# Kernel optimization log

Hardware: AMD Instinct MI355X
Metric: run time of the kernel (lower is better)

## Reference

```python
import jax, jax.numpy as jnp
import numpy as np

N = 20000        # atoms
NEIGH = 12       # neighbors per atom
BSTEPS = 40      # bond GBF steps, range [0, 8]
ASTEPS = 20      # angle GBF steps, range [-1, 1]
H = 64           # hidden size
NCLS = 2         # n_classification
NCRYS = 20       # crystals (contiguous blocks of 1000 atoms)
NREL = 3         # edge relation types


def gbf(data, dmin, dmax, steps):
    # Gaussian basis expansion: exp(-(d - mu)^2 / gamma^2), gamma = (max-min)/steps
    filters = jnp.linspace(dmin, dmax, steps)
    gamma = (dmax - dmin) / steps
    return jnp.exp(-((data[..., None] - filters) ** 2) / gamma ** 2)


def rgcn(x, src, dst, etype, W_rel, W_root, b):
    # RGCNConv (PyG default): out = x @ W_root + b + sum_r mean_{j in N_r(i)} x_j @ W_r
    out = x @ W_root + b
    for r in range(NREL):
        w = (etype == r).astype(x.dtype)                     # [E]
        msg = (x @ W_rel[r])[src] * w[:, None]               # transform-then-gather: [E, H]
        s = jax.ops.segment_sum(msg, dst, num_segments=x.shape[0])
        c = jax.ops.segment_sum(w, dst, num_segments=x.shape[0])
        out = out + s / jnp.maximum(c, 1.0)[:, None]
    return out


def _forward(bond_fea, angle_fea, species, nbr_idx, crys_idx,
             W1b_rel, W1b_root, b1b, W1a_rel, W1a_root, b1a,
             W2b_rel, W2b_root, b2b, W2a_rel, W2a_root, b2a,
             fc_W, fc_b):
    n = bond_fea.shape[0]
    src = jnp.repeat(jnp.arange(n, dtype=jnp.int32), NEIGH)  # edge sources
    dst = nbr_idx.reshape(-1)                                # edge targets
    etype = species[src] + species[dst]                      # 0/1/2 per species pair

    edge_fea = gbf(bond_fea, 0.0, 8.0, BSTEPS).reshape(n, -1)      # [N, 480]
    ang_fea = gbf(angle_fea, -1.0, 1.0, ASTEPS).reshape(n, -1)     # [N, 2880]

    bf = jax.nn.relu(rgcn(edge_fea, src, dst, etype, W1b_rel, W1b_root, b1b))
    af = jax.nn.relu(rgcn(ang_fea, src, dst, etype, W1a_rel, W1a_root, b1a))
    # dropout treated as identity (eval/deterministic reference)
    bf = jax.nn.relu(rgcn(bf, src, dst, etype, W2b_rel, W2b_root, b2b))
    af = jax.nn.relu(rgcn(af, src, dst, etype, W2a_rel, W2a_root, b2a))

    feat = jnp.concatenate([bf, af], axis=1)                 # [N, 128]

    # pool: mean over contiguous [start, end) ranges per crystal
    starts = crys_idx[:, 0]
    crys_id = jnp.searchsorted(starts, jnp.arange(n), side='right') - 1
    sums = jax.ops.segment_sum(feat, crys_id, num_segments=NCRYS)
    counts = (crys_idx[:, 1] - crys_idx[:, 0]).astype(feat.dtype)[:, None]
    pooled = sums / counts                                   # [NCRYS, 128]

    return pooled @ fc_W + fc_b                              # [NCRYS, NCLS]


def setup_inputs() -> dict:
    key = jax.random.key(0)
    ks = jax.random.split(key, 20)
    bond_fea = jax.random.uniform(ks[0], (N, NEIGH), dtype=jnp.float32) * 8.0
    angle_fea = jax.random.uniform(ks[1], (N, NEIGH, NEIGH), dtype=jnp.float32) * 2.0 - 1.0
    species = jax.random.randint(ks[2], (N,), 0, 2, dtype=jnp.int32)
    nbr_idx = jax.random.randint(ks[3], (N, NEIGH), 0, N, dtype=jnp.int32)
    starts = jnp.arange(NCRYS, dtype=jnp.int32) * (N // NCRYS)
    crys_idx = jnp.stack([starts, starts + (N // NCRYS)], axis=1)

    def w(k, shape, fan_in):
        return jax.random.normal(k, shape, dtype=jnp.float32) / np.sqrt(fan_in)

    in_b = BSTEPS * NEIGH            # 480
    in_a = ASTEPS * NEIGH * NEIGH    # 2880
    return {
        'bond_fea': bond_fea, 'angle_fea': angle_fea, 'species': species,
        'nbr_idx': nbr_idx, 'crys_idx': crys_idx,
        'W1b_rel': w(ks[4], (NREL, in_b, H), in_b), 'W1b_root': w(ks[5], (in_b, H), in_b),
        'b1b': jnp.zeros((H,), jnp.float32),
        'W1a_rel': w(ks[6], (NREL, in_a, H), in_a), 'W1a_root': w(ks[7], (in_a, H), in_a),
        'b1a': jnp.zeros((H,), jnp.float32),
        'W2b_rel': w(ks[8], (NREL, H, H), H), 'W2b_root': w(ks[9], (H, H), H),
        'b2b': jnp.zeros((H,), jnp.float32),
        'W2a_rel': w(ks[10], (NREL, H, H), H), 'W2a_root': w(ks[11], (H, H), H),
        'b2a': jnp.zeros((H,), jnp.float32),
        'fc_W': w(ks[12], (2 * H, NCLS), 2 * H), 'fc_b': jnp.zeros((NCLS,), jnp.float32),
    }


def reference(bond_fea, angle_fea, species, nbr_idx, crys_idx,
              W1b_rel, W1b_root, b1b, W1a_rel, W1a_root, b1a,
              W2b_rel, W2b_root, b2b, W2a_rel, W2a_root, b2a,
              fc_W, fc_b):
    return _forward(bond_fea, angle_fea, species, nbr_idx, crys_idx,
                    W1b_rel, W1b_root, b1b, W1a_rel, W1a_root, b1a,
                    W2b_rel, W2b_root, b2b, W2a_rel, W2a_root, b2a,
                    fc_W, fc_b)
```

## Files before the change

kernel.cpp:

```cpp
#include <hip/hip_runtime.h>

#define NN 20000
#define NNP 20096
#define NEIGH 12
#define NCRYS 20
#define MT2 1256
#define NSUB 16

typedef __bf16 bf16x8 __attribute__((ext_vector_type(8)));
typedef __bf16 bf16x4 __attribute__((ext_vector_type(4)));
typedef float f32x4 __attribute__((ext_vector_type(4)));

__device__ __forceinline__ void pack_one(const float* Wrel, const float* Wroot,
                                         __bf16* Wp, int K, int idx) {
    int k = idx >> 8, n = idx & 255;
    int r = n >> 6, h = n & 63;
    float v = (r < 3) ? Wrel[((size_t)r * K + k) * 64 + h] : Wroot[(size_t)k * 64 + h];
    int kt = k >> 5, k8 = (k >> 3) & 3, j = k & 7, nt = n >> 4, ni = n & 15;
    Wp[((((size_t)kt * 16 + nt) * 4 + k8) * 16 + ni) * 8 + j] = (__bf16)v;
}

__device__ __forceinline__ void pack_cat(const float* Wrel, const float* Wroot,
                                         __bf16* Wp, int idx) {
    int k4 = idx >> 6, n = idx & 63;
    int q = k4 >> 6, kk = k4 & 63;
    float v = q ? Wrel[(((q - 1) * 64 + kk) * 64) + n] : Wroot[kk * 64 + n];
    int kt = k4 >> 5, k8 = (k4 >> 3) & 3, j = k4 & 7, nt = n >> 4, ni = n & 15;
    Wp[((((size_t)kt * 4 + nt) * 4 + k8) * 16 + ni) * 8 + j] = (__bf16)v;
}

__global__ __launch_bounds__(256) void setup_kernel(
    const int* __restrict__ species, const int* __restrict__ nbr,
    int* __restrict__ adj, int* __restrict__ deg,
    const float* __restrict__ W1b_rel, const float* __restrict__ W1b_root,
    const float* __restrict__ W1a_rel, const float* __restrict__ W1a_root,
    const float* __restrict__ W2b_rel, const float* __restrict__ W2b_root,
    const float* __restrict__ W2a_rel, const float* __restrict__ W2a_root,
    __bf16* __restrict__ Wp1b, __bf16* __restrict__ Wp1a,
    __bf16* __restrict__ Wp2b, __bf16* __restrict__ Wp2a,
    const float* __restrict__ bond, const float* __restrict__ angle,
    float* __restrict__ bondT, float* __restrict__ angleT) {
    __shared__ float ls[64 * 145];
    const int bx = blockIdx.x, tid = threadIdx.x;
    if (bx < 938) {
        int e = bx * 256 + tid;
        if (e < NN * NEIGH) {
            int i = e / NEIGH;
            int d = nbr[e];
            int r = species[i] + species[d];
            int slot = atomicAdd(&deg[d], 1);
            if (slot < 64) adj[(size_t)d * 64 + slot] = i | (r << 28);
        }
    } else if (bx < 938 + 256) {
        const int S0 = 480 * 256;
        const int S1 = S0 + 2880 * 256;
        const int S2 = S1 + 16384;
        const int S3 = S2 + 16384;
        const int S4 = S3 + 8192;
        const int S5 = S4 + 49152;
        for (int idx = (bx - 938) * 256 + tid; idx < S5; idx += 256 * 256) {
            if (idx < S0)       pack_one(W1b_rel, W1b_root, Wp1b, 480, idx);
            else if (idx < S1)  pack_one(W1a_rel, W1a_root, Wp1a, 2880, idx - S0);
            else if (idx < S2)  pack_cat(W2b_rel, W2b_root, Wp2b, idx - S1);
            else if (idx < S3)  pack_cat(W2a_rel, W2a_root, Wp2a, idx - S2);
            else if (idx < S4)  Wp1b[480 * 256 + (idx - S3)] = (__bf16)0.f;
            else                Wp1a[2880 * 256 + (idx - S4)] = (__bf16)0.f;
        }
    } else {
        int tb = bx - 1194;
        if (tb < 314) {
            int m0 = tb * 64;
            for (int idx = tid; idx < 64 * 144; idx += 256) {
                int mm = idx / 144, j = idx - mm * 144;
                int m = m0 + mm;
                ls[mm * 145 + j] = (m < NN) ? angle[(size_t)m * 144 + j] : 0.f;
            }
            __syncthreads();
            for (int idx = tid; idx < 156 * 64; idx += 256) {
                int j = idx >> 6, mm = idx & 63;
                angleT[(size_t)j * NNP + m0 + mm] = (j < 144) ? ls[mm * 145 + j] : 0.f;
            }
        } else {
            int m0 = (tb - 314) * 64;
            for (int idx = tid; idx < 64 * 12; idx += 256) {
                int mm = idx / 12, j = idx - mm * 12;
                int m = m0 + mm;
                ls[mm * 13 + j] = (m < NN) ? bond[(size_t)m * 12 + j] : 0.f;
            }
            __syncthreads();
            for (int idx = tid; idx < 16 * 64; idx += 256) {
                int j = idx >> 6, mm = idx & 63;
                bondT[(size_t)j * NNP + m0 + mm] = (j < 12) ? ls[mm * 13 + j] : 0.f;
            }
        }
    }
}

template <int MODE, typename OUT_T>
__device__ __forceinline__ void gemm1_body(const float* __restrict__ xT,
                                           const __bf16* __restrict__ Wp,
                                           OUT_T* __restrict__ Y, int mb,
                                           __bf16* __restrict__ Al,
                                           int ph0, int nph) {
    constexpr int DIVN = (MODE == 0) ? 40 : 20;
    constexpr int ADDJ = 64 / DIVN;
    constexpr int ADDS = 64 % DIVN;
    constexpr float F0 = (MODE == 0) ? 0.f : -1.f;
    constexpr float FS = (MODE == 0) ? (8.f / 39.f) : (2.f / 19.f);
    constexpr float NG2 = ((MODE == 0) ? -25.f : -100.f) * 1.44269504f;
    const float C  = __builtin_amdgcn_exp2f(2.f * NG2 * FS * FS);
    const float P1 = NG2 * FS * FS;
    const float P2 = -2.f * NG2 * FS;

    const int tid = threadIdx.x;
    const int lane = tid & 63, wv = tid >> 6;
    const int m0 = mb * 64;
    const int smt = tid >> 7;
    const int sk8 = (tid >> 5) & 3;
    const int smi = (tid >> 1) & 15;
    const int sjh = (tid & 1) * 4;
    const int sgm = m0 + smt * 16 + smi;
    const int kk0 = sk8 * 8 + sjh;
    const int swoff = (((smt * 4 + sk8) * 16 + smi) * 8 + sjh);
    const int k8b = lane >> 4, nib = lane & 15;

    f32x4 acc[4][2] = {};

    const int k00 = ph0 * 64 + kk0;
    const int k01 = ph0 * 64 + 32 + kk0;
    const float* pA0 = xT + (size_t)(k00 / DIVN) * NNP + sgm;
    const float* pA1 = xT + (size_t)(k01 / DIVN) * NNP + sgm;
    int sL0 = k00 % DIVN, sL1 = k01 % DIVN;
    int sS0 = sL0, sS1 = sL1;

    const bf16x8* pB0 = (const bf16x8*)Wp + (size_t)ph0 * 2048 +
                        ((size_t)(2 * wv) * 4 + k8b) * 16 + nib;
    const bf16x8* pB1 = pB0 + 1024;

    bf16x8 bEv[4], bOd[4];

    auto advL = [&]() {
        sL0 += ADDS;
        if (sL0 >= DIVN) { sL0 -= DIVN; pA0 += (size_t)(ADDJ + 1) * NNP; } else pA0 += (size_t)ADDJ * NNP;
        sL1 += ADDS;
        if (sL1 >= DIVN) { sL1 -= DIVN; pA1 += (size_t)(ADDJ + 1) * NNP; } else pA1 += (size_t)ADDJ * NNP;
    };
    auto advS = [&]() {
        sS0 += ADDS; if (sS0 >= DIVN) sS0 -= DIVN;
        sS1 += ADDS; if (sS1 >= DIVN) sS1 -= DIVN;
    };
    auto loadB = [&](bf16x8* d) {
        d[0] = pB0[0]; d[1] = pB0[64]; d[2] = pB1[0]; d[3] = pB1[64];
        pB0 += 2048; pB1 += 2048;
    };
    auto stage = [&](float a0, float a1, __bf16* dst) {
        float d0 = a0 - (F0 + (float)sS0 * FS);
        float d1 = a1 - (F0 + (float)sS1 * FS);
        float e0a = __builtin_amdgcn_exp2f(NG2 * d0 * d0);
        float q0a = __builtin_amdgcn_exp2f(fmaf(P2, d0, P1));
        float e0b = __builtin_amdgcn_exp2f(NG2 * d1 * d1);
        float q0b = __builtin_amdgcn_exp2f(fmaf(P2, d1, P1));
        float e1a = e0a * q0a, q1a = q0a * C;
        float e2a = e1a * q1a, e3a = e2a * q1a * C;
        float e1b = e0b * q0b, q1b = q0b * C;
        float e2b = e1b * q1b, e3b = e2b * q1b * C;
        bf16x4 v0, v1;
        v0[0] = (__bf16)e0a; v0[1] = (__bf16)e1a; v0[2] = (__bf16)e2a; v0[3] = (__bf16)e3a;
        v1[0] = (__bf16)e0b; v1[1] = (__bf16)e1b; v1[2] = (__bf16)e2b; v1[3] = (__bf16)e3b;
        *(bf16x4*)&dst[swoff] = v0;
        *(bf16x4*)&dst[2048 + swoff] = v1;
    };
    auto mma = [&](const __bf16* Ab, const bf16x8* bc) {
        bf16x8 af[4], ag[4];
#pragma unroll
        for (int t4 = 0; t4 < 4; ++t4) {
            af[t4] = *(const bf16x8*)&Ab[(((((t4 << 2) + k8b) << 4) + nib) << 3)];
            ag[t4] = *(const bf16x8*)&Ab[2048 + (((((t4 << 2) + k8b) << 4) + nib) << 3)];
        }
#pragma unroll
        for (int i = 0; i < 4; ++i) {
            acc[i][0] = __builtin_amdgcn_mfma_f32_16x16x32_bf16(af[i], bc[0], acc[i][0], 0, 0, 0);
            acc[i][1] = __builtin_amdgcn_mfma_f32_16x16x32_bf16(af[i], bc[1], acc[i][1], 0, 0, 0);
        }
#pragma unroll
        for (int i = 0; i < 4; ++i) {
            acc[i][0] = __builtin_amdgcn_mfma_f32_16x16x32_bf16(ag[i], bc[2], acc[i][0], 0, 0, 0);
            acc[i][1] = __builtin_amdgcn_mfma_f32_16x16x32_bf16(ag[i], bc[3], acc[i][1], 0, 0, 0);
        }
    };

    float a00 = pA0[0], a01 = pA1[0]; advL();
    float aN0 = pA0[0], aN1 = pA1[0]; advL();
    stage(a00, a01, Al); advS();
    loadB(bEv);
    loadB(bOd);
    __syncthreads();

    const int np2 = nph >> 1;
    for (int p2 = 0; p2 < np2; ++p2) {
        const bool last = (p2 == np2 - 1);
        mma(Al, bEv);
        if (!last) loadB(bEv);
        stage(aN0, aN1, Al + 4096); advS();
        if (!last) { aN0 = pA0[0]; aN1 = pA1[0]; advL(); }
        __syncthreads();
        mma(Al + 4096, bOd);
        if (!last) {
            loadB(bOd);
            stage(aN0, aN1, Al); advS();
            aN0 = pA0[0]; aN1 = pA1[0]; advL();
        }
        __syncthreads();
    }

    const int mrow0 = m0 + ((lane >> 4) << 2);
    const int ncol = (wv << 5) + nib;
#pragma unroll
    for (int i = 0; i < 4; ++i)
#pragma unroll
        for (int j = 0; j < 2; ++j)
#pragma unroll
            for (int v = 0; v < 4; ++v) {
                int m = mrow0 + i * 16 + v;
                if (m < NN) Y[(size_t)m * 256 + ncol + j * 16] = (OUT_T)acc[i][j][v];
            }
}

__global__ __launch_bounds__(512, 4) void mega_gemm1(const float* __restrict__ bondT,
                                                     const float* __restrict__ angleT,
                                                     const __bf16* __restrict__ Wp1b,
                                                     const __bf16* __restrict__ Wp1a,
                                                     __bf16* __restrict__ Yb,
                                                     float* __restrict__ Ya1,
                                                     float* __restrict__ Ya2) {
    __shared__ __align__(16) __bf16 Al[2 * 4096];
    int bx = blockIdx.x;
    if (bx < 314)       gemm1_body<1, float>(angleT, Wp1a, Ya1, bx, Al, 0, 24);
    else if (bx < 628)  gemm1_body<1, float>(angleT, Wp1a, Ya2, bx - 314, Al, 24, 24);
    else                gemm1_body<0, __bf16>(bondT, Wp1b, Yb, bx - 628, Al, 0, 8);
}

__global__ __launch_bounds__(256) void addY(const float* __restrict__ Y1,
                                            const float* __restrict__ Y2,
                                            __bf16* __restrict__ Yo) {
    size_t i = ((size_t)blockIdx.x * 256 + threadIdx.x) * 8;
    f32x4 a0 = *(const f32x4*)&Y1[i], a1 = *(const f32x4*)&Y1[i + 4];
    f32x4 b0 = *(const f32x4*)&Y2[i], b1 = *(const f32x4*)&Y2[i + 4];
    bf16x8 o;
#pragma unroll
    for (int c = 0; c < 4; ++c) {
        o[c] = (__bf16)(a0[c] + b0[c]);
        o[4 + c] = (__bf16)(a1[c] + b1[c]);
    }
    *(bf16x8*)&Yo[i] = o;
}

__global__ __launch_bounds__(256) void agg1(const __bf16* __restrict__ Yb,
                                            const __bf16* __restrict__ Ya,
                                            const int* __restrict__ adj,
                                            const int* __restrict__ deg,
                                            const float* __restrict__ biasb,
                                            const float* __restrict__ biasa,
                                            __bf16* __restrict__ Hb,
                                            __bf16* __restrict__ Ha) {
    int node = blockIdx.x * 4 + (threadIdx.x >> 6);
    int h = threadIdx.x & 63;
    if (node >= NN) return;
    int dg = min(deg[node], 64);
    int e = adj[(size_t)node * 64 + h];
    bool val = h < dg;
    int r = e >> 28;
    unsigned long long bl0 = __ballot(val && r == 0);
    unsigned long long bl1 = __ballot(val && r == 1);
    unsigned long long bl2 = __ballot(val && r == 2);
    int c0 = __popcll(bl0), c1 = __popcll(bl1), c2 = __popcll(bl2);
    float sb0 = 0.f, sb1 = 0.f, sb2 = 0.f;
    float sa0 = 0.f, sa1 = 0.f, sa2 = 0.f;
    if (dg > 0) {
        int e0 = __builtin_amdgcn_readfirstlane(e);
        int ec = val ? e : e0;
        for (int k0 = 0; k0 < dg; k0 += 16) {
            float vb[16], va[16];
#pragma unroll
            for (int i = 0; i < 16; ++i) {
                int ek = __builtin_amdgcn_readlane(ec, k0 + i);
                size_t base = (size_t)(ek & 0x0FFFFFFF) * 256 + (ek >> 28) * 64 + h;
                vb[i] = (float)Yb[base];
                va[i] = (float)Ya[base];
            }
#pragma unroll
            for (int i = 0; i < 16; ++i) {
                int kk = k0 + i;
                if (kk < dg) {
                    int rr = __builtin_amdgcn_readlane(ec, kk) >> 28;
                    if (rr == 0)      { sb0 += vb[i]; sa0 += va[i]; }
                    else if (rr == 1) { sb1 += vb[i]; sa1 += va[i]; }
                    else              { sb2 += vb[i]; sa2 += va[i]; }
                }
            }
        }
    }
    float i0 = 1.f / fmaxf((float)c0, 1.f);
    float i1 = 1.f / fmaxf((float)c1, 1.f);
    float i2 = 1.f / fmaxf((float)c2, 1.f);
    float ob = (float)Yb[(size_t)node * 256 + 192 + h] + biasb[h] + sb0 * i0 + sb1 * i1 + sb2 * i2;
    float oa = (float)Ya[(size_t)node * 256 + 192 + h] + biasa[h] + sa0 * i0 + sa1 * i1 + sa2 * i2;
    Hb[(size_t)node * 64 + h] = (__bf16)fmaxf(ob, 0.f);
    Ha[(size_t)node * 64 + h] = (__bf16)fmaxf(oa, 0.f);
}

__global__ __launch_bounds__(256) void agg2(const __bf16* __restrict__ Hb,
                                            const __bf16* __restrict__ Ha,
                                            const int* __restrict__ adj,
                                            const int* __restrict__ deg,
                                            __bf16* __restrict__ Apb,
                                            __bf16* __restrict__ Apa) {
    int node = blockIdx.x * 4 + (threadIdx.x >> 6);
    int h = threadIdx.x & 63;
    float hb = 0.f, rb0 = 0.f, rb1 = 0.f, rb2 = 0.f;
    float ha = 0.f, ra0 = 0.f, ra1 = 0.f, ra2 = 0.f;
    if (node < NN) {
        int dg = min(deg[node], 64);
        int e = adj[(size_t)node * 64 + h];
        bool val = h < dg;
        int r = e >> 28;
        unsigned long long bl0 = __ballot(val && r == 0);
        unsigned long long bl1 = __ballot(val && r == 1);
        unsigned long long bl2 = __ballot(val && r == 2);
        int c0 = __popcll(bl0), c1 = __popcll(bl1), c2 = __popcll(bl2);
        float sb0 = 0.f, sb1 = 0.f, sb2 = 0.f;
        float sa0 = 0.f, sa1 = 0.f, sa2 = 0.f;
        hb = (float)Hb[(size_t)node * 64 + h];
        ha = (float)Ha[(size_t)node * 64 + h];
        if (dg > 0) {
            int e0 = __builtin_amdgcn_readfirstlane(e);
            int ec = val ? e : e0;
            for (int k0 = 0; k0 < dg; k0 += 16) {
                float vb[16], va[16];
#pragma unroll
                for (int i = 0; i < 16; ++i) {
                    int ek = __builtin_amdgcn_readlane(ec, k0 + i);
                    size_t base = (size_t)(ek & 0x0FFFFFFF) * 64 + h;
                    vb[i] = (float)Hb[base];
                    va[i] = (float)Ha[base];
                }
#pragma unroll
                for (int i = 0; i < 16; ++i) {
                    int kk = k0 + i;
                    if (kk < dg) {
                        int rr = __builtin_amdgcn_readlane(ec, kk) >> 28;
                        if (rr == 0)      { sb0 += vb[i]; sa0 += va[i]; }
                        else if (rr == 1) { sb1 += vb[i]; sa1 += va[i]; }
                        else              { sb2 += vb[i]; sa2 += va[i]; }
                    }
                }
            }
        }
        float i0 = 1.f / fmaxf((float)c0, 1.f);
        float i1 = 1.f / fmaxf((float)c1, 1.f);
        float i2 = 1.f / fmaxf((float)c2, 1.f);
        rb0 = sb0 * i0; rb1 = sb1 * i1; rb2 = sb2 * i2;
        ra0 = sa0 * i0; ra1 = sa1 * i1; ra2 = sa2 * i2;
    }
    int mt = node >> 4, mi = node & 15;
    float vb4[4] = {hb, rb0, rb1, rb2};
    float va4[4] = {ha, ra0, ra1, ra2};
#pragma unroll
    for (int q = 0; q < 4; ++q) {
        int K4 = q * 64 + h;
        int kt = K4 >> 5, k8 = (K4 >> 3) & 3, j = K4 & 7;
        size_t off = ((((size_t)kt * MT2 + mt) * 4 + k8) * 16 + mi) * 8 + j;
        Apb[off] = (__bf16)vb4[q];
        Apa[off] = (__bf16)va4[q];
    }
}

__global__ __launch_bounds__(256) void gemm3(const __bf16* __restrict__ Apb,
                                             const __bf16* __restrict__ Apa,
                                             const __bf16* __restrict__ Wpb,
                                             const __bf16* __restrict__ Wpa,
                                             const float* __restrict__ bb,
                                             const float* __restrict__ ba,
                                             const int* __restrict__ crys,
                                             float* __restrict__ pooled) {
    const int ch = blockIdx.y;
    const bf16x8* Ag = (const bf16x8*)(ch ? Apa : Apb);
    const bf16x8* Bg = (const bf16x8*)(ch ? Wpa : Wpb);
    const float* bias = ch ? ba : bb;
    const int base = ch ? 64 : 0;
    const int tid = threadIdx.x, lane = tid & 63, wv = tid >> 6;
    const int mt0 = blockIdx.x * 8 + wv * 2;
    const int k8b = lane >> 4, nib = lane & 15;
    f32x4 acc[2][4] = {};
#pragma unroll
    for (int kt = 0; kt < 8; ++kt) {
        bf16x8 a0 = Ag[(((size_t)kt * MT2 + mt0) * 4 + k8b) * 16 + nib];
        bf16x8 a1 = Ag[(((size_t)kt * MT2 + mt0 + 1) * 4 + k8b) * 16 + nib];
        bf16x8 b0 = Bg[(((size_t)kt * 4 + 0) * 4 + k8b) * 16 + nib];
        bf16x8 b1 = Bg[(((size_t)kt * 4 + 1) * 4 + k8b) * 16 + nib];
        bf16x8 b2 = Bg[(((size_t)kt * 4 + 2) * 4 + k8b) * 16 + nib];
        bf16x8 b3 = Bg[(((size_t)kt * 4 + 3) * 4 + k8b) * 16 + nib];
        acc[0][0] = __builtin_amdgcn_mfma_f32_16x16x32_bf16(a0, b0, acc[0][0], 0, 0, 0);
        acc[0][1] = __builtin_amdgcn_mfma_f32_16x16x32_bf16(a0, b1, acc[0][1], 0, 0, 0);
        acc[0][2] = __builtin_amdgcn_mfma_f32_16x16x32_bf16(a0, b2, acc[0][2], 0, 0, 0);
        acc[0][3] = __builtin_amdgcn_mfma_f32_16x16x32_bf16(a0, b3, acc[0][3], 0, 0, 0);
        acc[1][0] = __builtin_amdgcn_mfma_f32_16x16x32_bf16(a1, b0, acc[1][0], 0, 0, 0);
        acc[1][1] = __builtin_amdgcn_mfma_f32_16x16x32_bf16(a1, b1, acc[1][1], 0, 0, 0);
        acc[1][2] = __builtin_amdgcn_mfma_f32_16x16x32_bf16(a1, b2, acc[1][2], 0, 0, 0);
        acc[1][3] = __builtin_amdgcn_mfma_f32_16x16x32_bf16(a1, b3, acc[1][3], 0, 0, 0);
    }
    const int rowoff = ((lane >> 4) << 2);
#pragma unroll
    for (int i = 0; i < 2; ++i)
#pragma unroll
        for (int v = 0; v < 4; ++v) {
            int m = (mt0 + i) * 16 + rowoff + v;
            if (m < NN) {
                int cc = 0;
#pragma unroll
                for (int t = 1; t < NCRYS; ++t) cc += (m >= crys[t * 2]) ? 1 : 0;
                int sub = ((m >> 4) + ((m >> 2) & 3)) & (NSUB - 1);
                float* pb = &pooled[((size_t)cc * NSUB + sub) * 128 + base];
#pragma unroll
                for (int j = 0; j < 4; ++j) {
                    int n = j * 16 + nib;
                    float o = fmaxf(acc[i][j][v] + bias[n], 0.f);
                    atomicAdd(&pb[n], o);
                }
            }
        }
}

__global__ void final2(const float* __restrict__ pooled, const int* __restrict__ crys,
                       const float* __restrict__ fcW, const float* __restrict__ fcb,
                       float* __restrict__ out) {
    int c = blockIdx.x >> 1, o = blockIdx.x & 1;
    int l = threadIdx.x;
    float cnt = (float)(crys[c * 2 + 1] - crys[c * 2]);
    float sb = 0.f, sa = 0.f;
    for (int s = 0; s < NSUB; ++s) {
        sb += pooled[((size_t)c * NSUB + s) * 128 + l];
        sa += pooled[((size_t)c * NSUB + s) * 128 + 64 + l];
    }
    float a = sb * fcW[l * 2 + o] + sa * fcW[(64 + l) * 2 + o];
    for (int s = 32; s > 0; s >>= 1) a += __shfl_down(a, s);
    if (l == 0) out[c * 2 + o] = a / cnt + fcb[o];
}

extern "C" void kernel_launch(void* const* d_in, const int* in_sizes, int n_in,
                              void* d_out, int out_size, void* d_ws, size_t ws_size,
                              hipStream_t stream) {
    const float* bond    = (const float*)d_in[0];
    const float* angle   = (const float*)d_in[1];
    const int*   species = (const int*)d_in[2];
    const int*   nbr     = (const int*)d_in[3];
    const int*   crys    = (const int*)d_in[4];
    const float* W1b_rel = (const float*)d_in[5];
    const float* W1b_root= (const float*)d_in[6];
    const float* b1b     = (const float*)d_in[7];
    const float* W1a_rel = (const float*)d_in[8];
    const float* W1a_root= (const float*)d_in[9];
    const float* b1a     = (const float*)d_in[10];
    const float* W2b_rel = (const float*)d_in[11];
    const float* W2b_root= (const float*)d_in[12];
    const float* b2b     = (const float*)d_in[13];
    const float* W2a_rel = (const float*)d_in[14];
    const float* W2a_root= (const float*)d_in[15];
    const float* b2a     = (const float*)d_in[16];
    const float* fcW     = (const float*)d_in[17];
    const float* fcb     = (const float*)d_in[18];
    float* out = (float*)d_out;

    char* ws = (char*)d_ws;
    size_t off = 0;
    auto alloc = [&](size_t bytes) {
        char* p = ws + off;
        off = (off + bytes + 255) & ~(size_t)255;
        return p;
    };
    __bf16* Wp1b = (__bf16*)alloc((size_t)512 * 256 * 2);
    __bf16* Wp1a = (__bf16*)alloc((size_t)3072 * 256 * 2);
    __bf16* Wp2b = (__bf16*)alloc((size_t)256 * 64 * 2);
    __bf16* Wp2a = (__bf16*)alloc((size_t)256 * 64 * 2);
    float*  bondT = (float*)alloc((size_t)16 * NNP * 4);
    float*  angleT= (float*)alloc((size_t)156 * NNP * 4);
    __bf16* Yb   = (__bf16*)alloc((size_t)NN * 256 * 2);
    __bf16* Ya   = (__bf16*)alloc((size_t)NN * 256 * 2);
    float*  Ya1  = (float*)alloc((size_t)NN * 256 * 4);
    float*  Ya2  = (float*)alloc((size_t)NN * 256 * 4);
    __bf16* Hrowb= (__bf16*)alloc((size_t)NNP * 64 * 2);
    __bf16* Hrowa= (__bf16*)alloc((size_t)NNP * 64 * 2);
    __bf16* Apb  = (__bf16*)alloc((size_t)8 * MT2 * 512 * 2);
    __bf16* Apa  = (__bf16*)alloc((size_t)8 * MT2 * 512 * 2);
    int*    adj  = (int*)alloc((size_t)NN * 64 * 4);
    int*    deg  = (int*)alloc((size_t)NN * 4);
    float*  pooled = (float*)alloc((size_t)NCRYS * NSUB * 128 * 4);

    hipMemsetAsync(deg, 0, (size_t)NN * 4, stream);
    hipMemsetAsync(pooled, 0, (size_t)NCRYS * NSUB * 128 * 4, stream);

    setup_kernel<<<1822, 256, 0, stream>>>(species, nbr, adj, deg,
                                           W1b_rel, W1b_root, W1a_rel, W1a_root,
                                           W2b_rel, W2b_root, W2a_rel, W2a_root,
                                           Wp1b, Wp1a, Wp2b, Wp2a,
                                           bond, angle, bondT, angleT);

    mega_gemm1<<<942, 512, 0, stream>>>(bondT, angleT, Wp1b, Wp1a, Yb, Ya1, Ya2);
    addY<<<2500, 256, 0, stream>>>(Ya1, Ya2, Ya);
    agg1<<<5024, 256, 0, stream>>>(Yb, Ya, adj, deg, b1b, b1a, Hrowb, Hrowa);
    agg2<<<5024, 256, 0, stream>>>(Hrowb, Hrowa, adj, deg, Apb, Apa);
    gemm3<<<dim3(157, 2), 256, 0, stream>>>(Apb, Apa, Wp2b, Wp2a, b2b, b2a, crys, pooled);
    final2<<<NCRYS * 2, 64, 0, stream>>>(pooled, crys, fcW, fcb, out);
}
```

Baseline: 236.9 us.

## Fuse split-K reduction into GEMM via tickets, precompute edge weights, pool in LDS

Removes the separate addY kernel. The two split-K halves of the angle GEMM now pair up through a per-tile ticket and flag: the first block to finish writes fp32 partials, and the second spins until the flag is set, then adds the partials and writes bf16. agg1 computes per-edge mean weights once and stores them, so agg1 and agg2 use weighted FMAs with readlane instead of branchy per-relation accumulation. gemm3 first reduces pooled sums in shared memory per crystal before doing global atomics. The spin-wait depends on the partner block being resident, which risks deadlock or stalls.

```diff
diff --git a/kernel.cpp b/kernel.cpp
--- a/kernel.cpp
+++ b/kernel.cpp
@@ -10,6 +10,10 @@
 typedef __bf16 bf16x8 __attribute__((ext_vector_type(8)));
 typedef __bf16 bf16x4 __attribute__((ext_vector_type(4)));
 typedef float f32x4 __attribute__((ext_vector_type(4)));
+
+__device__ __forceinline__ float readlane_f(float v, int l) {
+    return __int_as_float(__builtin_amdgcn_readlane(__float_as_int(v), l));
+}
 
 __device__ __forceinline__ void pack_one(const float* Wrel, const float* Wroot,
                                          __bf16* Wp, int K, int idx) {
@@ -96,12 +100,11 @@
     }
 }
 
-template <int MODE, typename OUT_T>
-__device__ __forceinline__ void gemm1_body(const float* __restrict__ xT,
+template <int MODE>
+__device__ __forceinline__ void gemm1_core(const float* __restrict__ xT,
                                            const __bf16* __restrict__ Wp,
-                                           OUT_T* __restrict__ Y, int mb,
-                                           __bf16* __restrict__ Al,
-                                           int ph0, int nph) {
+                                           int mb, __bf16* __restrict__ Al,
+                                           int ph0, int nph, f32x4 (&acc)[4][2]) {
     constexpr int DIVN = (MODE == 0) ? 40 : 20;
     constexpr int ADDJ = 64 / DIVN;
     constexpr int ADDS = 64 % DIVN;
@@ -123,8 +126,6 @@
     const int kk0 = sk8 * 8 + sjh;
     const int swoff = (((smt * 4 + sk8) * 16 + smi) * 8 + sjh);
     const int k8b = lane >> 4, nib = lane & 15;
-
-    f32x4 acc[4][2] = {};
 
     const int k00 = ph0 * 64 + kk0;
     const int k01 = ph0 * 64 + 32 + kk0;
@@ -212,18 +213,6 @@
         }
         __syncthreads();
     }
-
-    const int mrow0 = m0 + ((lane >> 4) << 2);
-    const int ncol = (wv << 5) + nib;
-#pragma unroll
-    for (int i = 0; i < 4; ++i)
-#pragma unroll
-        for (int j = 0; j < 2; ++j)
-#pragma unroll
-            for (int v = 0; v < 4; ++v) {
-                int m = mrow0 + i * 16 + v;
-                if (m < NN) Y[(size_t)m * 256 + ncol + j * 16] = (OUT_T)acc[i][j][v];
-            }
 }
 
 __global__ __launch_bounds__(512, 4) void mega_gemm1(const float* __restrict__ bondT,
@@ -231,28 +220,71 @@
                                                      const __bf16* __restrict__ Wp1b,
                                                      const __bf16* __restrict__ Wp1a,
                                                      __bf16* __restrict__ Yb,
-                                                     float* __restrict__ Ya1,
-                                                     float* __restrict__ Ya2) {
+                                                     float* __restrict__ YaP,
+                                                     __bf16* __restrict__ Ya,
+                                                     int* __restrict__ tickets,
+                                                     int* __restrict__ flags) {
     __shared__ __align__(16) __bf16 Al[2 * 4096];
-    int bx = blockIdx.x;
-    if (bx < 314)       gemm1_body<1, float>(angleT, Wp1a, Ya1, bx, Al, 0, 24);
-    else if (bx < 628)  gemm1_body<1, float>(angleT, Wp1a, Ya2, bx - 314, Al, 24, 24);
-    else                gemm1_body<0, __bf16>(bondT, Wp1b, Yb, bx - 628, Al, 0, 8);
-}
-
-__global__ __launch_bounds__(256) void addY(const float* __restrict__ Y1,
-                                            const float* __restrict__ Y2,
-                                            __bf16* __restrict__ Yo) {
-    size_t i = ((size_t)blockIdx.x * 256 + threadIdx.x) * 8;
-    f32x4 a0 = *(const f32x4*)&Y1[i], a1 = *(const f32x4*)&Y1[i + 4];
-    f32x4 b0 = *(const f32x4*)&Y2[i], b1 = *(const f32x4*)&Y2[i + 4];
-    bf16x8 o;
-#pragma unroll
-    for (int c = 0; c < 4; ++c) {
-        o[c] = (__bf16)(a0[c] + b0[c]);
-        o[4 + c] = (__bf16)(a1[c] + b1[c]);
-    }
-    *(bf16x8*)&Yo[i] = o;
+    __shared__ int role;
+    const int bx = blockIdx.x;
+    const int tid = threadIdx.x;
+    const int lane = tid & 63, wv = tid >> 6;
+    f32x4 acc[4][2] = {};
+    if (bx < 628) {
+        const int half = (bx >= 314) ? 1 : 0;
+        const int mb = half ? bx - 314 : bx;
+        gemm1_core<1>(angleT, Wp1a, mb, Al, half ? 24 : 0, 24, acc);
+        const int mrow0 = mb * 64 + ((lane >> 4) << 2);
+        const int ncol = (wv << 5) + (lane & 15);
+        if (tid == 0) role = atomicAdd(&tickets[mb], 1);
+        __syncthreads();
+        if (role == 0) {
+#pragma unroll
+            for (int i = 0; i < 4; ++i)
+#pragma unroll
+                for (int j = 0; j < 2; ++j)
+#pragma unroll
+                    for (int v = 0; v < 4; ++v) {
+                        int m = mrow0 + i * 16 + v;
+                        if (m < NN) YaP[(size_t)m * 256 + ncol + j * 16] = acc[i][j][v];
+                    }
+            __threadfence();
+            __syncthreads();
+            if (tid == 0) atomicExch(&flags[mb], 1);
+        } else {
+            if (tid == 0) {
+                while (atomicAdd(&flags[mb], 0) == 0) __builtin_amdgcn_s_sleep(16);
+            }
+            __syncthreads();
+            __threadfence();
+#pragma unroll
+            for (int i = 0; i < 4; ++i)
+#pragma unroll
+                for (int j = 0; j < 2; ++j)
+#pragma unroll
+                    for (int v = 0; v < 4; ++v) {
+                        int m = mrow0 + i * 16 + v;
+                        if (m < NN) {
+                            size_t o = (size_t)m * 256 + ncol + j * 16;
+                            Ya[o] = (__bf16)(YaP[o] + acc[i][j][v]);
+                        }
+                    }
+        }
+    } else {
+        const int mb = bx - 628;
+        gemm1_core<0>(bondT, Wp1b, mb, Al, 0, 8, acc);
+        const int mrow0 = mb * 64 + ((lane >> 4) << 2);
+        const int ncol = (wv << 5) + (lane & 15);
+#pragma unroll
+        for (int i = 0; i < 4; ++i)
+#pragma unroll
+            for (int j = 0; j < 2; ++j)
+#pragma unroll
+                for (int v = 0; v < 4; ++v) {
+                    int m = mrow0 + i * 16 + v;
+                    if (m < NN) Yb[(size_t)m * 256 + ncol + j * 16] = (__bf16)acc[i][j][v];
+                }
+    }
 }
 
 __global__ __launch_bounds__(256) void agg1(const __bf16* __restrict__ Yb,
@@ -262,7 +294,8 @@
                                             const float* __restrict__ biasb,
                                             const float* __restrict__ biasa,
                                             __bf16* __restrict__ Hb,
-                                            __bf16* __restrict__ Ha) {
+                                            __bf16* __restrict__ Ha,
+                                            float* __restrict__ adjw) {
     int node = blockIdx.x * 4 + (threadIdx.x >> 6);
     int h = threadIdx.x & 63;
     if (node >= NN) return;
@@ -274,8 +307,10 @@
     unsigned long long bl1 = __ballot(val && r == 1);
     unsigned long long bl2 = __ballot(val && r == 2);
     int c0 = __popcll(bl0), c1 = __popcll(bl1), c2 = __popcll(bl2);
-    float sb0 = 0.f, sb1 = 0.f, sb2 = 0.f;
-    float sa0 = 0.f, sa1 = 0.f, sa2 = 0.f;
+    float w = 0.f;
+    if (val) w = 1.f / (float)((r == 0) ? c0 : (r == 1) ? c1 : c2);
+    adjw[(size_t)node * 64 + h] = w;
+    float sb = 0.f, sa = 0.f;
     if (dg > 0) {
         int e0 = __builtin_amdgcn_readfirstlane(e);
         int ec = val ? e : e0;
@@ -290,21 +325,14 @@
             }
 #pragma unroll
             for (int i = 0; i < 16; ++i) {
-                int kk = k0 + i;
-                if (kk < dg) {
-                    int rr = __builtin_amdgcn_readlane(ec, kk) >> 28;
-                    if (rr == 0)      { sb0 += vb[i]; sa0 += va[i]; }
-                    else if (rr == 1) { sb1 += vb[i]; sa1 += va[i]; }
-                    else              { sb2 += vb[i]; sa2 += va[i]; }
-                }
-            }
-        }
-    }
-    float i0 = 1.f / fmaxf((float)c0, 1.f);
-    float i1 = 1.f / fmaxf((float)c1, 1.f);
-    float i2 = 1.f / fmaxf((float)c2, 1.f);
-    float ob = (float)Yb[(size_t)node * 256 + 192 + h] + biasb[h] + sb0 * i0 + sb1 * i1 + sb2 * i2;
-    float oa = (float)Ya[(size_t)node * 256 + 192 + h] + biasa[h] + sa0 * i0 + sa1 * i1 + sa2 * i2;
+                float wk = readlane_f(w, k0 + i);
+                sb = fmaf(vb[i], wk, sb);
+                sa = fmaf(va[i], wk, sa);
+            }
+        }
+    }
+    float ob = (float)Yb[(size_t)node * 256 + 192 + h] + biasb[h] + sb;
+    float oa = (float)Ya[(size_t)node * 256 + 192 + h] + biasa[h] + sa;
     Hb[(size_t)node * 64 + h] = (__bf16)fmaxf(ob, 0.f);
     Ha[(size_t)node * 64 + h] = (__bf16)fmaxf(oa, 0.f);
 }
@@ -313,6 +341,7 @@
                                             const __bf16* __restrict__ Ha,
                                             const int* __restrict__ adj,
                                             const int* __restrict__ deg,
+                                            const float* __restrict__ adjw,
                                             __bf16* __restrict__ Apb,
                                             __bf16* __restrict__ Apa) {
     int node = blockIdx.x * 4 + (threadIdx.x >> 6);
@@ -323,13 +352,11 @@
         int dg = min(deg[node], 64);
         int e = adj[(size_t)node * 64 + h];
         bool val = h < dg;
+        float w = adjw[(size_t)node * 64 + h];
         int r = e >> 28;
-        unsigned long long bl0 = __ballot(val && r == 0);
-        unsigned long long bl1 = __ballot(val && r == 1);
-        unsigned long long bl2 = __ballot(val && r == 2);
-        int c0 = __popcll(bl0), c1 = __popcll(bl1), c2 = __popcll(bl2);
-        float sb0 = 0.f, sb1 = 0.f, sb2 = 0.f;
-        float sa0 = 0.f, sa1 = 0.f, sa2 = 0.f;
+        float w0 = (r == 0) ? w : 0.f;
+        float w1 = (r == 1) ? w : 0.f;
+        float w2 = (r == 2) ? w : 0.f;
         hb = (float)Hb[(size_t)node * 64 + h];
         ha = (float)Ha[(size_t)node * 64 + h];
         if (dg > 0) {
@@ -346,21 +373,15 @@
                 }
 #pragma unroll
                 for (int i = 0; i < 16; ++i) {
-                    int kk = k0 + i;
-                    if (kk < dg) {
-                        int rr = __builtin_amdgcn_readlane(ec, kk) >> 28;
-                        if (rr == 0)      { sb0 += vb[i]; sa0 += va[i]; }
-                        else if (rr == 1) { sb1 += vb[i]; sa1 += va[i]; }
-                        else              { sb2 += vb[i]; sa2 += va[i]; }
-                    }
+                    float wk0 = readlane_f(w0, k0 + i);
+                    float wk1 = readlane_f(w1, k0 + i);
+                    float wk2 = readlane_f(w2, k0 + i);
+                    rb0 = fmaf(vb[i], wk0, rb0); ra0 = fmaf(va[i], wk0, ra0);
+                    rb1 = fmaf(vb[i], wk1, rb1); ra1 = fmaf(va[i], wk1, ra1);
+                    rb2 = fmaf(vb[i], wk2, rb2); ra2 = fmaf(va[i], wk2, ra2);
                 }
             }
         }
-        float i0 = 1.f / fmaxf((float)c0, 1.f);
-        float i1 = 1.f / fmaxf((float)c1, 1.f);
-        float i2 = 1.f / fmaxf((float)c2, 1.f);
-        rb0 = sb0 * i0; rb1 = sb1 * i1; rb2 = sb2 * i2;
-        ra0 = sa0 * i0; ra1 = sa1 * i1; ra2 = sa2 * i2;
     }
     int mt = node >> 4, mi = node & 15;
     float vb4[4] = {hb, rb0, rb1, rb2};
@@ -383,6 +404,7 @@
                                              const float* __restrict__ ba,
                                              const int* __restrict__ crys,
                                              float* __restrict__ pooled) {
+    __shared__ float lpool[2][64];
     const int ch = blockIdx.y;
     const bf16x8* Ag = (const bf16x8*)(ch ? Apa : Apb);
     const bf16x8* Bg = (const bf16x8*)(ch ? Wpa : Wpb);
@@ -391,6 +413,7 @@
     const int tid = threadIdx.x, lane = tid & 63, wv = tid >> 6;
     const int mt0 = blockIdx.x * 8 + wv * 2;
     const int k8b = lane >> 4, nib = lane & 15;
+    if (tid < 128) ((float*)lpool)[tid] = 0.f;
     f32x4 acc[2][4] = {};
 #pragma unroll
     for (int kt = 0; kt < 8; ++kt) {
@@ -409,6 +432,11 @@
         acc[1][2] = __builtin_amdgcn_mfma_f32_16x16x32_bf16(a1, b2, acc[1][2], 0, 0, 0);
         acc[1][3] = __builtin_amdgcn_mfma_f32_16x16x32_bf16(a1, b3, acc[1][3], 0, 0, 0);
     }
+    const int node0 = blockIdx.x * 128;
+    int cbase = 0;
+#pragma unroll
+    for (int t = 1; t < NCRYS; ++t) cbase += (node0 >= crys[t * 2]) ? 1 : 0;
+    __syncthreads();
     const int rowoff = ((lane >> 4) << 2);
 #pragma unroll
     for (int i = 0; i < 2; ++i)
@@ -419,16 +447,25 @@
                 int cc = 0;
 #pragma unroll
                 for (int t = 1; t < NCRYS; ++t) cc += (m >= crys[t * 2]) ? 1 : 0;
-                int sub = ((m >> 4) + ((m >> 2) & 3)) & (NSUB - 1);
-                float* pb = &pooled[((size_t)cc * NSUB + sub) * 128 + base];
+                int locc = cc - cbase;
 #pragma unroll
                 for (int j = 0; j < 4; ++j) {
                     int n = j * 16 + nib;
                     float o = fmaxf(acc[i][j][v] + bias[n], 0.f);
-                    atomicAdd(&pb[n], o);
+                    atomicAdd(&lpool[locc][n], o);
                 }
             }
         }
+    __syncthreads();
+    if (tid < 128) {
+        int locc = tid >> 6, n = tid & 63;
+        float vsum = lpool[locc][n];
+        int cc = cbase + locc;
+        if (vsum != 0.f && cc < NCRYS) {
+            int sub = blockIdx.x & (NSUB - 1);
+            atomicAdd(&pooled[((size_t)cc * NSUB + sub) * 128 + base + n], vsum);
+        }
+    }
 }
 
 __global__ void final2(const float* __restrict__ pooled, const int* __restrict__ crys,
@@ -486,17 +523,19 @@
     float*  angleT= (float*)alloc((size_t)156 * NNP * 4);
     __bf16* Yb   = (__bf16*)alloc((size_t)NN * 256 * 2);
     __bf16* Ya   = (__bf16*)alloc((size_t)NN * 256 * 2);
-    float*  Ya1  = (float*)alloc((size_t)NN * 256 * 4);
-    float*  Ya2  = (float*)alloc((size_t)NN * 256 * 4);
+    float*  YaP  = (float*)alloc((size_t)NN * 256 * 4);
     __bf16* Hrowb= (__bf16*)alloc((size_t)NNP * 64 * 2);
     __bf16* Hrowa= (__bf16*)alloc((size_t)NNP * 64 * 2);
     __bf16* Apb  = (__bf16*)alloc((size_t)8 * MT2 * 512 * 2);
     __bf16* Apa  = (__bf16*)alloc((size_t)8 * MT2 * 512 * 2);
+    float*  adjw = (float*)alloc((size_t)NN * 64 * 4);
     int*    adj  = (int*)alloc((size_t)NN * 64 * 4);
-    int*    deg  = (int*)alloc((size_t)NN * 4);
+    int*    deg  = (int*)alloc((size_t)(NN + 640) * 4);
+    int*    tickets = deg + NN;
+    int*    flags   = deg + NN + 314;
     float*  pooled = (float*)alloc((size_t)NCRYS * NSUB * 128 * 4);
 
-    hipMemsetAsync(deg, 0, (size_t)NN * 4, stream);
+    hipMemsetAsync(deg, 0, (size_t)(NN + 640) * 4, stream);
     hipMemsetAsync(pooled, 0, (size_t)NCRYS * NSUB * 128 * 4, stream);
 
     setup_kernel<<<1822, 256, 0, stream>>>(species, nbr, adj, deg,
@@ -505,10 +544,9 @@
                                            Wp1b, Wp1a, Wp2b, Wp2a,
                                            bond, angle, bondT, angleT);
 
-    mega_gemm1<<<942, 512, 0, stream>>>(bondT, angleT, Wp1b, Wp1a, Yb, Ya1, Ya2);
-    addY<<<2500, 256, 0, stream>>>(Ya1, Ya2, Ya);
-    agg1<<<5024, 256, 0, stream>>>(Yb, Ya, adj, deg, b1b, b1a, Hrowb, Hrowa);
-    agg2<<<5024, 256, 0, stream>>>(Hrowb, Hrowa, adj, deg, Apb, Apa);
+    mega_gemm1<<<942, 512, 0, stream>>>(bondT, angleT, Wp1b, Wp1a, Yb, YaP, Ya, tickets, flags);
+    agg1<<<5024, 256, 0, stream>>>(Yb, Ya, adj, deg, b1b, b1a, Hrowb, Hrowa, adjw);
+    agg2<<<5024, 256, 0, stream>>>(Hrowb, Hrowa, adj, deg, adjw, Apb, Apa);
     gemm3<<<dim3(157, 2), 256, 0, stream>>>(Apb, Apa, Wp2b, Wp2a, b2b, b2a, crys, pooled);
     final2<<<NCRYS * 2, 64, 0, stream>>>(pooled, crys, fcW, fcb, out);
 }
```

Measured after the change: 382.2 us. +61.3%, slower.

## Vectorize agg1 gathers, precompute mean weights, pool gemm3 outputs in shared memory

Applied to the files above, without the earlier changes.

agg1 now has each lane load four bf16 features at once, covering four edges per step across lane groups, and folds the per-relation mean weight into an FMA. It also writes per-edge normalization weights that agg2 reuses, so agg2 no longer needs ballots or relation branching. gemm3 accumulates pooled sums in shared memory per block and issues one global atomic per crystal and channel, instead of one per element. The changes add an extra buffer of per-edge weights plus a cross-lane reduction, and the local pooling assumes a 128-node block spans at most two crystals.

```diff
diff --git a/kernel.cpp b/kernel.cpp
--- a/kernel.cpp
+++ b/kernel.cpp
@@ -10,6 +10,10 @@
 typedef __bf16 bf16x8 __attribute__((ext_vector_type(8)));
 typedef __bf16 bf16x4 __attribute__((ext_vector_type(4)));
 typedef float f32x4 __attribute__((ext_vector_type(4)));
+
+__device__ __forceinline__ float readlane_f(float v, int l) {
+    return __int_as_float(__builtin_amdgcn_readlane(__float_as_int(v), l));
+}
 
 __device__ __forceinline__ void pack_one(const float* Wrel, const float* Wroot,
                                          __bf16* Wp, int K, int idx) {
@@ -262,57 +266,79 @@
                                             const float* __restrict__ biasb,
                                             const float* __restrict__ biasa,
                                             __bf16* __restrict__ Hb,
-                                            __bf16* __restrict__ Ha) {
+                                            __bf16* __restrict__ Ha,
+                                            float* __restrict__ adjw) {
     int node = blockIdx.x * 4 + (threadIdx.x >> 6);
-    int h = threadIdx.x & 63;
+    int lane = threadIdx.x & 63;
     if (node >= NN) return;
+    const int eg = lane >> 4, hq = lane & 15;
     int dg = min(deg[node], 64);
-    int e = adj[(size_t)node * 64 + h];
-    bool val = h < dg;
+    int e = adj[(size_t)node * 64 + lane];
+    bool val = lane < dg;
     int r = e >> 28;
     unsigned long long bl0 = __ballot(val && r == 0);
     unsigned long long bl1 = __ballot(val && r == 1);
     unsigned long long bl2 = __ballot(val && r == 2);
     int c0 = __popcll(bl0), c1 = __popcll(bl1), c2 = __popcll(bl2);
-    float sb0 = 0.f, sb1 = 0.f, sb2 = 0.f;
-    float sa0 = 0.f, sa1 = 0.f, sa2 = 0.f;
-    if (dg > 0) {
-        int e0 = __builtin_amdgcn_readfirstlane(e);
-        int ec = val ? e : e0;
-        for (int k0 = 0; k0 < dg; k0 += 16) {
-            float vb[16], va[16];
-#pragma unroll
-            for (int i = 0; i < 16; ++i) {
-                int ek = __builtin_amdgcn_readlane(ec, k0 + i);
-                size_t base = (size_t)(ek & 0x0FFFFFFF) * 256 + (ek >> 28) * 64 + h;
-                vb[i] = (float)Yb[base];
-                va[i] = (float)Ya[base];
-            }
-#pragma unroll
-            for (int i = 0; i < 16; ++i) {
-                int kk = k0 + i;
-                if (kk < dg) {
-                    int rr = __builtin_amdgcn_readlane(ec, kk) >> 28;
-                    if (rr == 0)      { sb0 += vb[i]; sa0 += va[i]; }
-                    else if (rr == 1) { sb1 += vb[i]; sa1 += va[i]; }
-                    else              { sb2 += vb[i]; sa2 += va[i]; }
-                }
-            }
-        }
-    }
-    float i0 = 1.f / fmaxf((float)c0, 1.f);
-    float i1 = 1.f / fmaxf((float)c1, 1.f);
-    float i2 = 1.f / fmaxf((float)c2, 1.f);
-    float ob = (float)Yb[(size_t)node * 256 + 192 + h] + biasb[h] + sb0 * i0 + sb1 * i1 + sb2 * i2;
-    float oa = (float)Ya[(size_t)node * 256 + 192 + h] + biasa[h] + sa0 * i0 + sa1 * i1 + sa2 * i2;
-    Hb[(size_t)node * 64 + h] = (__bf16)fmaxf(ob, 0.f);
-    Ha[(size_t)node * 64 + h] = (__bf16)fmaxf(oa, 0.f);
+    float w = 0.f;
+    if (val) w = 1.f / (float)((r == 0) ? c0 : (r == 1) ? c1 : c2);
+    adjw[(size_t)node * 64 + lane] = w;
+
+    int e0 = __builtin_amdgcn_readfirstlane(e);
+    int ec = val ? e : e0;
+
+    f32x4 sb = {0.f, 0.f, 0.f, 0.f}, sa = {0.f, 0.f, 0.f, 0.f};
+    for (int k0 = 0; k0 < dg; k0 += 16) {
+        int ek[4]; float wk[4];
+        bf16x4 vb[4], va[4];
+#pragma unroll
+        for (int t = 0; t < 4; ++t) {
+            int k = k0 + t * 4 + eg;
+            ek[t] = __shfl(ec, k);
+            wk[t] = __shfl(w, k);
+        }
+#pragma unroll
+        for (int t = 0; t < 4; ++t) {
+            size_t base = (size_t)(ek[t] & 0x0FFFFFFF) * 256 + ((ek[t] >> 28) << 6) + hq * 4;
+            vb[t] = *(const bf16x4*)(Yb + base);
+            va[t] = *(const bf16x4*)(Ya + base);
+        }
+#pragma unroll
+        for (int t = 0; t < 4; ++t)
+#pragma unroll
+            for (int j = 0; j < 4; ++j) {
+                sb[j] = fmaf((float)vb[t][j], wk[t], sb[j]);
+                sa[j] = fmaf((float)va[t][j], wk[t], sa[j]);
+            }
+    }
+#pragma unroll
+    for (int j = 0; j < 4; ++j) {
+        sb[j] += __shfl_xor(sb[j], 16);
+        sb[j] += __shfl_xor(sb[j], 32);
+        sa[j] += __shfl_xor(sa[j], 16);
+        sa[j] += __shfl_xor(sa[j], 32);
+    }
+    bf16x4 rb = *(const bf16x4*)(Yb + (size_t)node * 256 + 192 + hq * 4);
+    bf16x4 ra = *(const bf16x4*)(Ya + (size_t)node * 256 + 192 + hq * 4);
+    f32x4 bb4 = *(const f32x4*)(biasb + hq * 4);
+    f32x4 ba4 = *(const f32x4*)(biasa + hq * 4);
+    if (eg == 0) {
+        bf16x4 ob, oa;
+#pragma unroll
+        for (int j = 0; j < 4; ++j) {
+            ob[j] = (__bf16)fmaxf((float)rb[j] + bb4[j] + sb[j], 0.f);
+            oa[j] = (__bf16)fmaxf((float)ra[j] + ba4[j] + sa[j], 0.f);
+        }
+        *(bf16x4*)(Hb + (size_t)node * 64 + hq * 4) = ob;
+        *(bf16x4*)(Ha + (size_t)node * 64 + hq * 4) = oa;
+    }
 }
 
 __global__ __launch_bounds__(256) void agg2(const __bf16* __restrict__ Hb,
                                             const __bf16* __restrict__ Ha,
                                             const int* __restrict__ adj,
                                             const int* __restrict__ deg,
+                                            const float* __restrict__ adjw,
                                             __bf16* __restrict__ Apb,
                                             __bf16* __restrict__ Apa) {
     int node = blockIdx.x * 4 + (threadIdx.x >> 6);
@@ -323,13 +349,11 @@
         int dg = min(deg[node], 64);
         int e = adj[(size_t)node * 64 + h];
         bool val = h < dg;
+        float w = adjw[(size_t)node * 64 + h];
         int r = e >> 28;
-        unsigned long long bl0 = __ballot(val && r == 0);
-        unsigned long long bl1 = __ballot(val && r == 1);
-        unsigned long long bl2 = __ballot(val && r == 2);
-        int c0 = __popcll(bl0), c1 = __popcll(bl1), c2 = __popcll(bl2);
-        float sb0 = 0.f, sb1 = 0.f, sb2 = 0.f;
-        float sa0 = 0.f, sa1 = 0.f, sa2 = 0.f;
+        float w0 = (r == 0) ? w : 0.f;
+        float w1 = (r == 1) ? w : 0.f;
+        float w2 = (r == 2) ? w : 0.f;
         hb = (float)Hb[(size_t)node * 64 + h];
         ha = (float)Ha[(size_t)node * 64 + h];
         if (dg > 0) {
@@ -346,21 +370,15 @@
                 }
 #pragma unroll
                 for (int i = 0; i < 16; ++i) {
-                    int kk = k0 + i;
-                    if (kk < dg) {
-                        int rr = __builtin_amdgcn_readlane(ec, kk) >> 28;
-                        if (rr == 0)      { sb0 += vb[i]; sa0 += va[i]; }
-                        else if (rr == 1) { sb1 += vb[i]; sa1 += va[i]; }
-                        else              { sb2 += vb[i]; sa2 += va[i]; }
-                    }
+                    float wk0 = readlane_f(w0, k0 + i);
+                    float wk1 = readlane_f(w1, k0 + i);
+                    float wk2 = readlane_f(w2, k0 + i);
+                    rb0 = fmaf(vb[i], wk0, rb0); ra0 = fmaf(va[i], wk0, ra0);
+                    rb1 = fmaf(vb[i], wk1, rb1); ra1 = fmaf(va[i], wk1, ra1);
+                    rb2 = fmaf(vb[i], wk2, rb2); ra2 = fmaf(va[i], wk2, ra2);
                 }
             }
         }
-        float i0 = 1.f / fmaxf((float)c0, 1.f);
-        float i1 = 1.f / fmaxf((float)c1, 1.f);
-        float i2 = 1.f / fmaxf((float)c2, 1.f);
-        rb0 = sb0 * i0; rb1 = sb1 * i1; rb2 = sb2 * i2;
-        ra0 = sa0 * i0; ra1 = sa1 * i1; ra2 = sa2 * i2;
     }
     int mt = node >> 4, mi = node & 15;
     float vb4[4] = {hb, rb0, rb1, rb2};
@@ -383,6 +401,7 @@
                                              const float* __restrict__ ba,
                                              const int* __restrict__ crys,
                                              float* __restrict__ pooled) {
+    __shared__ float lpool[2][64];
     const int ch = blockIdx.y;
     const bf16x8* Ag = (const bf16x8*)(ch ? Apa : Apb);
     const bf16x8* Bg = (const bf16x8*)(ch ? Wpa : Wpb);
@@ -391,6 +410,7 @@
     const int tid = threadIdx.x, lane = tid & 63, wv = tid >> 6;
     const int mt0 = blockIdx.x * 8 + wv * 2;
     const int k8b = lane >> 4, nib = lane & 15;
+    if (tid < 128) ((float*)lpool)[tid] = 0.f;
     f32x4 acc[2][4] = {};
 #pragma unroll
     for (int kt = 0; kt < 8; ++kt) {
@@ -409,6 +429,11 @@
         acc[1][2] = __builtin_amdgcn_mfma_f32_16x16x32_bf16(a1, b2, acc[1][2], 0, 0, 0);
         acc[1][3] = __builtin_amdgcn_mfma_f32_16x16x32_bf16(a1, b3, acc[1][3], 0, 0, 0);
     }
+    const int node0 = blockIdx.x * 128;
+    int cbase = 0;
+#pragma unroll
+    for (int t = 1; t < NCRYS; ++t) cbase += (node0 >= crys[t * 2]) ? 1 : 0;
+    __syncthreads();
     const int rowoff = ((lane >> 4) << 2);
 #pragma unroll
     for (int i = 0; i < 2; ++i)
@@ -419,16 +444,25 @@
                 int cc = 0;
 #pragma unroll
                 for (int t = 1; t < NCRYS; ++t) cc += (m >= crys[t * 2]) ? 1 : 0;
-                int sub = ((m >> 4) + ((m >> 2) & 3)) & (NSUB - 1);
-                float* pb = &pooled[((size_t)cc * NSUB + sub) * 128 + base];
+                int locc = cc - cbase;
 #pragma unroll
                 for (int j = 0; j < 4; ++j) {
                     int n = j * 16 + nib;
                     float o = fmaxf(acc[i][j][v] + bias[n], 0.f);
-                    atomicAdd(&pb[n], o);
+                    atomicAdd(&lpool[locc][n], o);
                 }
             }
         }
+    __syncthreads();
+    if (tid < 128) {
+        int locc = tid >> 6, n = tid & 63;
+        float vsum = lpool[locc][n];
+        int cc = cbase + locc;
+        if (vsum != 0.f && cc < NCRYS) {
+            int sub = blockIdx.x & (NSUB - 1);
+            atomicAdd(&pooled[((size_t)cc * NSUB + sub) * 128 + base + n], vsum);
+        }
+    }
 }
 
 __global__ void final2(const float* __restrict__ pooled, const int* __restrict__ crys,
@@ -492,6 +526,7 @@
     __bf16* Hrowa= (__bf16*)alloc((size_t)NNP * 64 * 2);
     __bf16* Apb  = (__bf16*)alloc((size_t)8 * MT2 * 512 * 2);
     __bf16* Apa  = (__bf16*)alloc((size_t)8 * MT2 * 512 * 2);
+    float*  adjw = (float*)alloc((size_t)NN * 64 * 4);
     int*    adj  = (int*)alloc((size_t)NN * 64 * 4);
     int*    deg  = (int*)alloc((size_t)NN * 4);
     float*  pooled = (float*)alloc((size_t)NCRYS * NSUB * 128 * 4);
@@ -507,8 +542,8 @@
 
     mega_gemm1<<<942, 512, 0, stream>>>(bondT, angleT, Wp1b, Wp1a, Yb, Ya1, Ya2);
     addY<<<2500, 256, 0, stream>>>(Ya1, Ya2, Ya);
-    agg1<<<5024, 256, 0, stream>>>(Yb, Ya, adj, deg, b1b, b1a, Hrowb, Hrowa);
-    agg2<<<5024, 256, 0, stream>>>(Hrowb, Hrowa, adj, deg, Apb, Apa);
+    agg1<<<5024, 256, 0, stream>>>(Yb, Ya, adj, deg, b1b, b1a, Hrowb, Hrowa, adjw);
+    agg2<<<5024, 256, 0, stream>>>(Hrowb, Hrowa, adj, deg, adjw, Apb, Apa);
     gemm3<<<dim3(157, 2), 256, 0, stream>>>(Apb, Apa, Wp2b, Wp2a, b2b, b2a, crys, pooled);
     final2<<<NCRYS * 2, 64, 0, stream>>>(pooled, crys, fcW, fcb, out);
 }
```

New measurement: 248.5 us. 4.9% more time.
